# Kernel optimization log

Hardware: AMD Instinct MI355X
Metric: run time of the kernel (lower is better)

## Reference

```python
import jax, jax.numpy as jnp
import numpy as np

N, E, IN, H, C, ED = 100000, 1600000, 128, 4, 32, 16
HC = H * C
NEG_SLOPE = 0.2
EPS = 1e-5


def setup_inputs() -> dict:
    key = jax.random.key(0)
    ks = jax.random.split(key, 12)
    x = jax.random.normal(ks[0], (N, IN), jnp.float32)
    edge_index = jax.random.randint(ks[1], (2, E), 0, N, dtype=jnp.int32)
    edge_attr = jax.random.normal(ks[2], (E, ED), jnp.float32)
    s_in = 1.0 / np.sqrt(IN)
    s_ed = 1.0 / np.sqrt(ED)
    s_c = 1.0 / np.sqrt(C)
    Wl = jax.random.normal(ks[3], (IN, HC), jnp.float32) * s_in
    bl = jnp.zeros((HC,), jnp.float32)
    Wr = jax.random.normal(ks[4], (IN, HC), jnp.float32) * s_in
    br = jnp.zeros((HC,), jnp.float32)
    We = jax.random.normal(ks[5], (ED, HC), jnp.float32) * s_ed
    att = jax.random.normal(ks[6], (H, C), jnp.float32) * s_c
    bias = jnp.zeros((HC,), jnp.float32)
    ln_weight = jnp.ones((HC,), jnp.float32)
    ln_bias = jnp.zeros((HC,), jnp.float32)
    return {"x": x, "edge_index": edge_index, "edge_attr": edge_attr,
            "Wl": Wl, "bl": bl, "Wr": Wr, "br": br, "We": We,
            "att": att, "bias": bias, "ln_weight": ln_weight, "ln_bias": ln_bias}


def gatv2_block(x, src, dst, edge_attr, Wl, bl, Wr, br, We, att, bias, ln_weight, ln_bias):
    n = x.shape[0]
    xl = (x @ Wl + bl).reshape(n, H, C)  # source-side transform
    xr = (x @ Wr + br).reshape(n, H, C)  # target-side transform
    # add_self_loops with fill_value='mean': self-loop edge_attr = mean of
    # incoming edge_attr per node (0 for isolated nodes)
    ea_sum = jax.ops.segment_sum(edge_attr, dst, num_segments=n)
    cnt = jax.ops.segment_sum(jnp.ones((edge_attr.shape[0],), edge_attr.dtype), dst, num_segments=n)
    self_attr = ea_sum / jnp.maximum(cnt, 1.0)[:, None]
    loop = jnp.arange(n, dtype=src.dtype)
    src_a = jnp.concatenate([src, loop])
    dst_a = jnp.concatenate([dst, loop])
    ea_a = jnp.concatenate([edge_attr, self_attr], axis=0)
    e_emb = (ea_a @ We).reshape(-1, H, C)
    # GATv2 attention: a^T LeakyReLU(xl_j + xr_i + e)
    m = xl[src_a] + xr[dst_a] + e_emb            # [Etot, H, C]
    m = jax.nn.leaky_relu(m, NEG_SLOPE)
    alpha = jnp.einsum('ehc,hc->eh', m, att)     # [Etot, H]
    amax = jax.ops.segment_max(alpha, dst_a, num_segments=n)
    alpha = jnp.exp(alpha - amax[dst_a])
    denom = jax.ops.segment_sum(alpha, dst_a, num_segments=n)
    alpha = alpha / denom[dst_a]
    out = jax.ops.segment_sum(xl[src_a] * alpha[:, :, None], dst_a, num_segments=n)
    h = out.reshape(n, HC) + bias
    # residual (in_dim == H*C so no projection), PyG graph-mode LayerNorm
    z = x + h
    mu = jnp.mean(z)
    var = jnp.mean((z - mu) ** 2)
    z = (z - mu) / jnp.sqrt(var + EPS)
    z = z * ln_weight + ln_bias
    return jax.nn.relu(z)  # dropout = identity in eval


def reference(x, edge_index, edge_attr, Wl, bl, Wr, br, We, att, bias, ln_weight, ln_bias):
    src, dst = edge_index[0], edge_index[1]
    return gatv2_block(x, src, dst, edge_attr, Wl, bl, Wr, br, We, att, bias, ln_weight, ln_bias)
```

## Files before the change

kernel.cpp:

```cpp
#include <hip/hip_runtime.h>
#include <hip/hip_bf16.h>

static constexpr float NEG_SLOPE = 0.2f;
static constexpr float LN_EPS = 1e-5f;

typedef float v2f __attribute__((ext_vector_type(2)));
typedef __attribute__((ext_vector_type(8))) short bf16x8;
typedef __attribute__((ext_vector_type(4))) float f32x4;

__device__ __forceinline__ unsigned f2b(float f) {
  unsigned u = __float_as_uint(f);
  return (u + 0x7fffu + ((u >> 16) & 1u)) >> 16;
}
__device__ __forceinline__ v2f b2f2(ushort2 u) {
  v2f r;
  r.x = __uint_as_float((unsigned)u.x << 16);
  r.y = __uint_as_float((unsigned)u.y << 16);
  return r;
}
__device__ __forceinline__ float sbl(unsigned w) {
  return __uint_as_float(w << 16);
}
__device__ __forceinline__ float sbh(unsigned w) {
  return __uint_as_float(w & 0xFFFF0000u);
}

__device__ __forceinline__ float head_sum16(float x) {
  float t;
  t = __int_as_float(__builtin_amdgcn_update_dpp(
      0, __float_as_int(x), 0xB1, 0xF, 0xF, true));
  x += t;
  t = __int_as_float(__builtin_amdgcn_update_dpp(
      0, __float_as_int(x), 0x4E, 0xF, 0xF, true));
  x += t;
  t = __int_as_float(__builtin_amdgcn_update_dpp(
      0, __float_as_int(x), 0x124, 0xF, 0xF, true));
  x += t;
  t = __int_as_float(__builtin_amdgcn_update_dpp(
      0, __float_as_int(x), 0x128, 0xF, 0xF, true));
  x += t;
  return x;
}

__global__ __launch_bounds__(256) void k_packB(
    const float* __restrict__ Wl, const float* __restrict__ Wr,
    const float* __restrict__ bl, const float* __restrict__ br,
    ushort* __restrict__ Bpack, float* __restrict__ bcat,
    int* __restrict__ degcur, int N2, int* __restrict__ tot,
    int* __restrict__ src_pad, double* __restrict__ red)
{
  int tid = blockIdx.x * 256 + threadIdx.x;
  int l = tid & 63, s = (tid >> 6) & 3, t = tid >> 8;
  int col = t * 16 + (l & 15);
  int kb = s * 32 + (l >> 4) * 8;
  const float* __restrict__ W = (col < 128) ? Wl : Wr;
  int c = col & 127;
  unsigned p[4];
#pragma unroll
  for (int i = 0; i < 4; ++i) {
    unsigned lo = f2b(W[(size_t)(kb + 2 * i) * 128 + c]);
    unsigned hi = f2b(W[(size_t)(kb + 2 * i + 1) * 128 + c]);
    p[i] = lo | (hi << 16);
  }
  *(uint4*)(Bpack + (size_t)tid * 8) = make_uint4(p[0], p[1], p[2], p[3]);
  if (tid < 256) bcat[tid] = (tid < 128) ? bl[tid] : br[tid - 128];
  if (tid < 8) src_pad[tid] = 0;
  if (tid < 2) red[tid] = 0.0;
  if (tid == 0) *tot = 0;
  for (int i = tid; i < N2; i += 4096) degcur[i] = 0;
}

__global__ __launch_bounds__(256) void k_gemm_mfma(
    const float* __restrict__ x, const ushort* __restrict__ Bpack,
    const float* __restrict__ bcat, ushort* __restrict__ xl,
    float* __restrict__ outz, int n, const int* __restrict__ dst,
    int* __restrict__ deg, int E)
{
  const int lane = threadIdx.x & 63;
  const int w = threadIdx.x >> 6;
  const int row0 = blockIdx.x * 64 + w * 16;
  const int rowA = min(row0 + (lane & 15), n - 1);
  const int kgrp = lane >> 4;

  f32x4 acc[16];
#pragma unroll
  for (int t = 0; t < 16; ++t) acc[t] = (f32x4){0.f, 0.f, 0.f, 0.f};

#pragma unroll
  for (int s = 0; s < 4; ++s) {
    const float4* ap =
        (const float4*)(x + (size_t)rowA * 128 + s * 32 + kgrp * 8);
    float4 a0 = ap[0], a1 = ap[1];
    bf16x8 a;
    a[0] = (short)f2b(a0.x); a[1] = (short)f2b(a0.y);
    a[2] = (short)f2b(a0.z); a[3] = (short)f2b(a0.w);
    a[4] = (short)f2b(a1.x); a[5] = (short)f2b(a1.y);
    a[6] = (short)f2b(a1.z); a[7] = (short)f2b(a1.w);
#pragma unroll
    for (int t = 0; t < 16; ++t) {
      bf16x8 b =
          *(const bf16x8*)(Bpack + (((size_t)t * 4 + s) * 64 + lane) * 8);
      acc[t] = __builtin_amdgcn_mfma_f32_16x16x32_bf16(a, b, acc[t], 0, 0, 0);
    }
  }

  const int colg = lane & 15;
  const int rbase = row0 + (lane >> 4) * 4;
#pragma unroll
  for (int t = 0; t < 16; ++t) {
    const int col = t * 16 + colg;
    const float bia = bcat[col];
    if (col < 128) {
#pragma unroll
      for (int r = 0; r < 4; ++r) {
        const int R = rbase + r;
        if (R < n) xl[(size_t)R * 128 + col] = (ushort)f2b(acc[t][r] + bia);
      }
    } else {
      const int c = col - 128;
#pragma unroll
      for (int r = 0; r < 4; ++r) {
        const int R = rbase + r;
        if (R < n) outz[(size_t)R * 128 + c] = acc[t][r] + bia;
      }
    }
  }

  for (int e = blockIdx.x * 256 + threadIdx.x; e < E; e += gridDim.x * 256)
    atomicAdd(&deg[dst[e]], 1);
}

__global__ __launch_bounds__(256) void k_allocscan(
    const int* __restrict__ deg, int* __restrict__ offs, int* __restrict__ tot,
    int n)
{
  __shared__ int s[256];
  __shared__ int base;
  const int b = blockIdx.x, t = threadIdx.x, i = b * 256 + t;
  const int v = (i < n) ? deg[i] : 0;
  s[t] = v;
  __syncthreads();
  for (int o = 1; o < 256; o <<= 1) {
    int u = (t >= o) ? s[t - o] : 0;
    __syncthreads();
    s[t] += u;
    __syncthreads();
  }
  if (t == 255) base = atomicAdd(tot, s[255]);
  __syncthreads();
  if (i < n) offs[i] = base + s[t] - v;
}

__global__ __launch_bounds__(256) void k_fill(
    const int* __restrict__ src, const int* __restrict__ dst,
    const int* __restrict__ offs, int* __restrict__ cursor,
    const float4* __restrict__ ea4, int* __restrict__ csr_src,
    ushort* __restrict__ csr_ea, int E)
{
  int e = blockIdx.x * 256 + threadIdx.x;
  if (e >= E) return;
  int d = dst[e];
  int pos = offs[d] + atomicAdd(&cursor[d], 1);
  csr_src[pos] = src[e];
  float4 r0 = ea4[(size_t)e * 4 + 0], r1 = ea4[(size_t)e * 4 + 1];
  float4 r2 = ea4[(size_t)e * 4 + 2], r3 = ea4[(size_t)e * 4 + 3];
  uint4* o4 = (uint4*)(csr_ea + (size_t)pos * 16);
  o4[0] = make_uint4(f2b(r0.x) | (f2b(r0.y) << 16), f2b(r0.z) | (f2b(r0.w) << 16),
                     f2b(r1.x) | (f2b(r1.y) << 16), f2b(r1.z) | (f2b(r1.w) << 16));
  o4[1] = make_uint4(f2b(r2.x) | (f2b(r2.y) << 16), f2b(r2.z) | (f2b(r2.w) << 16),
                     f2b(r3.x) | (f2b(r3.y) << 16), f2b(r3.z) | (f2b(r3.w) << 16));
}

__global__ __launch_bounds__(256) void k_fused(
    const int* __restrict__ csr_src, const ushort* __restrict__ csr_ea,
    const int* __restrict__ offs, const int* __restrict__ deg,
    const ushort* __restrict__ xl, const float* __restrict__ We,
    const float* __restrict__ att, const float* __restrict__ x,
    const float* __restrict__ bias, float* __restrict__ outz,
    double* __restrict__ red, int N)
{
  const int lane = threadIdx.x & 63;
  const int wv = threadIdx.x >> 6;
  const int gw = __builtin_amdgcn_readfirstlane(blockIdx.x * 4 + wv);
  const int nw = gridDim.x * 4;
  const uint* __restrict__ eaD = (const uint*)csr_ea;
  const v2f* __restrict__ We2 = (const v2f*)We;
  const v2f* __restrict__ X2 = (const v2f*)x;
  v2f* __restrict__ Z2 = (v2f*)outz;

  __shared__ float sEA[4][2][256];
  float* const myEA = &sEA[wv][0][0];

  v2f we[16];
#pragma unroll
  for (int k = 0; k < 16; ++k) we[k] = We2[k * 64 + lane];
  const v2f a2 = ((const v2f*)att)[lane];
  const v2f b2 = ((const v2f*)bias)[lane];

  float sred = 0.f, s2red = 0.f;

  int node = gw;
  int beg = 0, len = 0;
  if (node < N) {
    beg = offs[node];
    len = deg[node];
  }
  uint d0 = 0, d1 = 0;
  if (node < N && len > 0) {
    const uint* p = eaD + (size_t)beg * 8;
    d0 = p[lane];
    d1 = p[lane + 64];
  }

  while (node < N) {
    const int nodeN = node + nw;
    int begN = 0, lenN = 0;
    if (nodeN < N) {
      begN = offs[nodeN];
      lenN = deg[nodeN];
    }

    const v2f xrv = Z2[(size_t)node * 64 + lane];
    const v2f xvSelf =
        b2f2(*(const ushort2*)(xl + (size_t)node * 128 + 2 * lane));

    float den = 0.f;
    v2f acc = {0.f, 0.f}, embsum = {0.f, 0.f};

    int buf = 0;
    if (len > 0) {
      float2* dst = (float2*)myEA;
      dst[lane] = make_float2(sbl(d0), sbh(d0));
      dst[lane + 64] = make_float2(sbl(d1), sbh(d1));
    }
    const int nchunk = (len + 15) >> 4;

    int g = beg;
    v2f xvCur = {0.f, 0.f};
    int sN = 0;
    if (len > 0) {
      const int s0 = csr_src[beg];
      xvCur = b2f2(*(const ushort2*)(xl + (size_t)s0 * 128 + 2 * lane));
      sN = csr_src[beg + 1];
    }

    for (int c = 0; c < nchunk; ++c) {
      if (c + 1 < nchunk) {
        const uint* p = eaD + (size_t)(beg + (c + 1) * 16) * 8;
        d0 = p[lane];
        d1 = p[lane + 64];
      } else if (nodeN < N && lenN > 0) {
        const uint* p = eaD + (size_t)begN * 8;
        d0 = p[lane];
        d1 = p[lane + 64];
      }
      const int m = min(16, len - c * 16);
      const float* eb = myEA + buf * 256;
      for (int i = 0; i < m; ++i) {
        const float4 q0 = *(const float4*)(eb + i * 16);
        const float4 q1 = *(const float4*)(eb + i * 16 + 4);
        const float4 q2 = *(const float4*)(eb + i * 16 + 8);
        const float4 q3 = *(const float4*)(eb + i * 16 + 12);
        const v2f xvN =
            b2f2(*(const ushort2*)(xl + (size_t)sN * 128 + 2 * lane));
        const int sNN = csr_src[g + 2];
        v2f u0 = q0.x * we[0];
        v2f u1 = q0.y * we[1];
        v2f u2 = q0.z * we[2];
        v2f u3 = q0.w * we[3];
        u0 += q1.x * we[4];
        u1 += q1.y * we[5];
        u2 += q1.z * we[6];
        u3 += q1.w * we[7];
        u0 += q2.x * we[8];
        u1 += q2.y * we[9];
        u2 += q2.z * we[10];
        u3 += q2.w * we[11];
        u0 += q3.x * we[12];
        u1 += q3.y * we[13];
        u2 += q3.z * we[14];
        u3 += q3.w * we[15];
        const v2f emb = (u0 + u1) + (u2 + u3);
        embsum += emb;
        v2f mm = xvCur + xrv + emb;
        v2f ml;
        ml.x = fmaxf(mm.x, NEG_SLOPE * mm.x);
        ml.y = fmaxf(mm.y, NEG_SLOPE * mm.y);
        const float part = head_sum16(fmaf(ml.y, a2.y, ml.x * a2.x));
        const float p = __expf(part);
        den += p;
        acc += xvCur * p;
        xvCur = xvN;
        sN = sNN;
        ++g;
      }
      if (c + 1 < nchunk) {
        float2* dst = (float2*)(myEA + (buf ^ 1) * 256);
        dst[lane] = make_float2(sbl(d0), sbh(d0));
        dst[lane + 64] = make_float2(sbl(d1), sbh(d1));
        buf ^= 1;
      }
    }
    if (nchunk == 0 && nodeN < N && lenN > 0) {
      const uint* p = eaD + (size_t)begN * 8;
      d0 = p[lane];
      d1 = p[lane + 64];
    }

    {
      const float inv = (len > 0) ? 1.f / (float)len : 0.f;
      const v2f embS = embsum * inv;
      v2f mm = xvSelf + xrv + embS;
      v2f ml;
      ml.x = fmaxf(mm.x, NEG_SLOPE * mm.x);
      ml.y = fmaxf(mm.y, NEG_SLOPE * mm.y);
      const float part = head_sum16(fmaf(ml.y, a2.y, ml.x * a2.x));
      const float p = __expf(part);
      den += p;
      acc += xvSelf * p;
    }

    const float invden = 1.f / den;
    const float o0 = acc.x * invden;
    const float o1 = acc.y * invden;

    const v2f xvn = X2[(size_t)node * 64 + lane];
    const float v0 = xvn.x + o0 + b2.x;
    const float v1 = xvn.y + o1 + b2.y;
    Z2[(size_t)node * 64 + lane] = (v2f){v0, v1};
    sred += v0 + v1;
    s2red += v0 * v0 + v1 * v1;

    node = nodeN;
    beg = begN;
    len = lenN;
  }

#pragma unroll
  for (int o = 32; o > 0; o >>= 1) {
    sred += __shfl_down(sred, o);
    s2red += __shfl_down(s2red, o);
  }
  __shared__ double ls[4], ls2[4];
  if ((threadIdx.x & 63) == 0) {
    ls[wv] = (double)sred;
    ls2[wv] = (double)s2red;
  }
  __syncthreads();
  if (threadIdx.x == 0) {
    unsafeAtomicAdd(red, ls[0] + ls[1] + ls[2] + ls[3]);
    unsafeAtomicAdd(red + 1, ls2[0] + ls2[1] + ls2[2] + ls2[3]);
  }
}

__global__ __launch_bounds__(256) void k_final(
    float* __restrict__ z, const double* __restrict__ red,
    const float* __restrict__ lnw, const float* __restrict__ lnb, int M4)
{
  int i = blockIdx.x * 256 + threadIdx.x;
  if (i >= M4) return;
  const double invM = 1.0 / ((double)M4 * 4.0);
  const double mu = red[0] * invM;
  const double var = red[1] * invM - mu * mu;
  const float sc = rsqrtf((float)var + LN_EPS);
  const float muf = (float)mu;
  const float4* W4 = (const float4*)lnw;
  const float4* L4 = (const float4*)lnb;
  float4* Z4 = (float4*)z;
  float4 zv = Z4[i], wv = W4[i & 31], lv = L4[i & 31];
  float4 o;
  o.x = fmaxf((zv.x - muf) * sc * wv.x + lv.x, 0.f);
  o.y = fmaxf((zv.y - muf) * sc * wv.y + lv.y, 0.f);
  o.z = fmaxf((zv.z - muf) * sc * wv.z + lv.z, 0.f);
  o.w = fmaxf((zv.w - muf) * sc * wv.w + lv.w, 0.f);
  Z4[i] = o;
}

extern "C" void kernel_launch(void* const* d_in, const int* in_sizes, int n_in,
                              void* d_out, int out_size, void* d_ws,
                              size_t ws_size, hipStream_t stream)
{
  const float* x = (const float*)d_in[0];
  const int* ei = (const int*)d_in[1];
  const float* edge_attr = (const float*)d_in[2];
  const float* Wl = (const float*)d_in[3];
  const float* bl = (const float*)d_in[4];
  const float* Wr = (const float*)d_in[5];
  const float* br = (const float*)d_in[6];
  const float* We = (const float*)d_in[7];
  const float* att = (const float*)d_in[8];
  const float* bias = (const float*)d_in[9];
  const float* lnw = (const float*)d_in[10];
  const float* lnb = (const float*)d_in[11];
  float* out = (float*)d_out;

  const int N = in_sizes[0] / 128;
  const int E = in_sizes[1] / 2;
  const int M = N * 128;
  const int* srcp = ei;
  const int* dstp = ei + E;
  const int nb = (N + 255) / 256;

  ushort* xl = (ushort*)d_ws;
  int* deg = (int*)(xl + (size_t)M);
  int* cursor = deg + N;
  int* offs = cursor + N;
  int* tot = offs + N;
  int* csr_src = tot + 8;
  ushort* csr_ea =
      (ushort*)((((size_t)(csr_src + E + 8)) + 63) & ~(size_t)63);
  double* red = (double*)(
      (((size_t)(csr_ea + (size_t)E * 16 + 512)) + 127) & ~(size_t)127);
  ushort* Bpack = (ushort*)(red + 8);
  float* bcat = (float*)(Bpack + 4096 * 8);

  k_packB<<<16, 256, 0, stream>>>(Wl, Wr, bl, br, Bpack, bcat, deg, 2 * N,
                                  tot, csr_src + E, red);
  k_gemm_mfma<<<(N + 63) / 64, 256, 0, stream>>>(x, Bpack, bcat, xl, out, N,
                                                 dstp, deg, E);
  k_allocscan<<<nb, 256, 0, stream>>>(deg, offs, tot, N);
  k_fill<<<(E + 255) / 256, 256, 0, stream>>>(srcp, dstp, offs, cursor,
                                              (const float4*)edge_attr,
                                              csr_src, csr_ea, E);
  k_fused<<<2048, 256, 0, stream>>>(csr_src, csr_ea, offs, deg, xl, We, att,
                                    x, bias, out, red, N);
  k_final<<<(M / 4 + 255) / 256, 256, 0, stream>>>(out, red, lnw, lnb, M / 4);
}
```

Before: 493.3 us.

## Compute edge embeddings with bf16 MFMA over padded 16-edge CSR chunks

Pads each node's CSR segment to a multiple of 16 and stores edge attributes in MFMA A-fragment layout. The fused kernel then computes each chunk's 16x128 edge embedding with bf16 MFMA into LDS instead of per-edge scalar FMAs. The source-row prefetch is also deepened to two edges ahead. This costs extra padded storage, a memset of the CSR buffers, and an LDS round trip, and it wastes half the MFMA K dimension.

```diff
diff --git a/kernel.cpp b/kernel.cpp
--- a/kernel.cpp
+++ b/kernel.cpp
@@ -17,12 +17,6 @@
   r.x = __uint_as_float((unsigned)u.x << 16);
   r.y = __uint_as_float((unsigned)u.y << 16);
   return r;
-}
-__device__ __forceinline__ float sbl(unsigned w) {
-  return __uint_as_float(w << 16);
-}
-__device__ __forceinline__ float sbh(unsigned w) {
-  return __uint_as_float(w & 0xFFFF0000u);
 }
 
 __device__ __forceinline__ float head_sum16(float x) {
@@ -47,7 +41,7 @@
     const float* __restrict__ bl, const float* __restrict__ br,
     ushort* __restrict__ Bpack, float* __restrict__ bcat,
     int* __restrict__ degcur, int N2, int* __restrict__ tot,
-    int* __restrict__ src_pad, double* __restrict__ red)
+    double* __restrict__ red)
 {
   int tid = blockIdx.x * 256 + threadIdx.x;
   int l = tid & 63, s = (tid >> 6) & 3, t = tid >> 8;
@@ -64,7 +58,6 @@
   }
   *(uint4*)(Bpack + (size_t)tid * 8) = make_uint4(p[0], p[1], p[2], p[3]);
   if (tid < 256) bcat[tid] = (tid < 128) ? bl[tid] : br[tid - 128];
-  if (tid < 8) src_pad[tid] = 0;
   if (tid < 2) red[tid] = 0.0;
   if (tid == 0) *tot = 0;
   for (int i = tid; i < N2; i += 4096) degcur[i] = 0;
@@ -137,7 +130,7 @@
   __shared__ int s[256];
   __shared__ int base;
   const int b = blockIdx.x, t = threadIdx.x, i = b * 256 + t;
-  const int v = (i < n) ? deg[i] : 0;
+  const int v = (i < n) ? ((deg[i] + 15) & ~15) : 0;
   s[t] = v;
   __syncthreads();
   for (int o = 1; o < 256; o <<= 1) {
@@ -155,7 +148,7 @@
     const int* __restrict__ src, const int* __restrict__ dst,
     const int* __restrict__ offs, int* __restrict__ cursor,
     const float4* __restrict__ ea4, int* __restrict__ csr_src,
-    ushort* __restrict__ csr_ea, int E)
+    uint4* __restrict__ csr_ea4, int E)
 {
   int e = blockIdx.x * 256 + threadIdx.x;
   if (e >= E) return;
@@ -164,11 +157,13 @@
   csr_src[pos] = src[e];
   float4 r0 = ea4[(size_t)e * 4 + 0], r1 = ea4[(size_t)e * 4 + 1];
   float4 r2 = ea4[(size_t)e * 4 + 2], r3 = ea4[(size_t)e * 4 + 3];
-  uint4* o4 = (uint4*)(csr_ea + (size_t)pos * 16);
-  o4[0] = make_uint4(f2b(r0.x) | (f2b(r0.y) << 16), f2b(r0.z) | (f2b(r0.w) << 16),
-                     f2b(r1.x) | (f2b(r1.y) << 16), f2b(r1.z) | (f2b(r1.w) << 16));
-  o4[1] = make_uint4(f2b(r2.x) | (f2b(r2.y) << 16), f2b(r2.z) | (f2b(r2.w) << 16),
-                     f2b(r3.x) | (f2b(r3.y) << 16), f2b(r3.z) | (f2b(r3.w) << 16));
+  const int chunk = pos >> 4, r = pos & 15;
+  csr_ea4[(size_t)chunk * 32 + r] =
+      make_uint4(f2b(r0.x) | (f2b(r0.y) << 16), f2b(r0.z) | (f2b(r0.w) << 16),
+                 f2b(r1.x) | (f2b(r1.y) << 16), f2b(r1.z) | (f2b(r1.w) << 16));
+  csr_ea4[(size_t)chunk * 32 + r + 16] =
+      make_uint4(f2b(r2.x) | (f2b(r2.y) << 16), f2b(r2.z) | (f2b(r2.w) << 16),
+                 f2b(r3.x) | (f2b(r3.y) << 16), f2b(r3.z) | (f2b(r3.w) << 16));
 }
 
 __global__ __launch_bounds__(256) void k_fused(
@@ -183,17 +178,28 @@
   const int wv = threadIdx.x >> 6;
   const int gw = __builtin_amdgcn_readfirstlane(blockIdx.x * 4 + wv);
   const int nw = gridDim.x * 4;
-  const uint* __restrict__ eaD = (const uint*)csr_ea;
-  const v2f* __restrict__ We2 = (const v2f*)We;
   const v2f* __restrict__ X2 = (const v2f*)x;
   v2f* __restrict__ Z2 = (v2f*)outz;
 
-  __shared__ float sEA[4][2][256];
-  float* const myEA = &sEA[wv][0][0];
-
-  v2f we[16];
-#pragma unroll
-  for (int k = 0; k < 16; ++k) we[k] = We2[k * 64 + lane];
+  __shared__ float sEmb[4][16 * 128];
+  float* const myEmb = sEmb[wv];
+
+  bf16x8 weB[8];
+  {
+    const int colb = lane & 15;
+    const int k0 = (lane >> 4) * 8;
+#pragma unroll
+    for (int t = 0; t < 8; ++t) {
+      bf16x8 b;
+#pragma unroll
+      for (int i = 0; i < 8; ++i) {
+        const int k = k0 + i;
+        b[i] = (k < 16) ? (short)f2b(We[(size_t)k * 128 + t * 16 + colb])
+                        : (short)0;
+      }
+      weB[t] = b;
+    }
+  }
   const v2f a2 = ((const v2f*)att)[lane];
   const v2f b2 = ((const v2f*)bias)[lane];
 
@@ -205,12 +211,9 @@
     beg = offs[node];
     len = deg[node];
   }
-  uint d0 = 0, d1 = 0;
-  if (node < N && len > 0) {
-    const uint* p = eaD + (size_t)beg * 8;
-    d0 = p[lane];
-    d1 = p[lane + 64];
-  }
+  uint4 afrag = {0, 0, 0, 0};
+  if (node < N && len > 0 && lane < 32)
+    afrag = *(const uint4*)(csr_ea + ((size_t)(beg >> 4) * 32 + lane) * 8);
 
   while (node < N) {
     const int nodeN = node + nw;
@@ -226,91 +229,72 @@
 
     float den = 0.f;
     v2f acc = {0.f, 0.f}, embsum = {0.f, 0.f};
-
-    int buf = 0;
+    const int nchunk = (len + 15) >> 4;
+    const int c0 = beg >> 4;
+
+    int g = beg;
+    v2f xv0 = {0.f, 0.f}, xv1 = {0.f, 0.f};
+    int s2 = 0;
     if (len > 0) {
-      float2* dst = (float2*)myEA;
-      dst[lane] = make_float2(sbl(d0), sbh(d0));
-      dst[lane + 64] = make_float2(sbl(d1), sbh(d1));
-    }
-    const int nchunk = (len + 15) >> 4;
-
-    int g = beg;
-    v2f xvCur = {0.f, 0.f};
-    int sN = 0;
-    if (len > 0) {
-      const int s0 = csr_src[beg];
-      xvCur = b2f2(*(const ushort2*)(xl + (size_t)s0 * 128 + 2 * lane));
-      sN = csr_src[beg + 1];
+      const int sa = csr_src[beg];
+      xv0 = b2f2(*(const ushort2*)(xl + (size_t)sa * 128 + 2 * lane));
+      const int sb = csr_src[beg + 1];
+      xv1 = b2f2(*(const ushort2*)(xl + (size_t)sb * 128 + 2 * lane));
+      s2 = csr_src[beg + 2];
     }
 
     for (int c = 0; c < nchunk; ++c) {
-      if (c + 1 < nchunk) {
-        const uint* p = eaD + (size_t)(beg + (c + 1) * 16) * 8;
-        d0 = p[lane];
-        d1 = p[lane + 64];
-      } else if (nodeN < N && lenN > 0) {
-        const uint* p = eaD + (size_t)begN * 8;
-        d0 = p[lane];
-        d1 = p[lane + 64];
+      uint4 afragN = {0, 0, 0, 0};
+      if (lane < 32) {
+        if (c + 1 < nchunk)
+          afragN =
+              *(const uint4*)(csr_ea + ((size_t)(c0 + c + 1) * 32 + lane) * 8);
+        else if (lenN > 0)
+          afragN =
+              *(const uint4*)(csr_ea + ((size_t)(begN >> 4) * 32 + lane) * 8);
+      }
+      {
+        const int colb = lane & 15;
+        const int row4 = (lane >> 4) * 4;
+        const bf16x8 a = *(const bf16x8*)&afrag;
+#pragma unroll
+        for (int t = 0; t < 8; ++t) {
+          f32x4 cf = __builtin_amdgcn_mfma_f32_16x16x32_bf16(
+              a, weB[t], (f32x4){0.f, 0.f, 0.f, 0.f}, 0, 0, 0);
+#pragma unroll
+          for (int q = 0; q < 4; ++q)
+            myEmb[(row4 + q) * 128 + t * 16 + colb] = cf[q];
+        }
       }
       const int m = min(16, len - c * 16);
-      const float* eb = myEA + buf * 256;
       for (int i = 0; i < m; ++i) {
-        const float4 q0 = *(const float4*)(eb + i * 16);
-        const float4 q1 = *(const float4*)(eb + i * 16 + 4);
-        const float4 q2 = *(const float4*)(eb + i * 16 + 8);
-        const float4 q3 = *(const float4*)(eb + i * 16 + 12);
-        const v2f xvN =
-            b2f2(*(const ushort2*)(xl + (size_t)sN * 128 + 2 * lane));
-        const int sNN = csr_src[g + 2];
-        v2f u0 = q0.x * we[0];
-        v2f u1 = q0.y * we[1];
-        v2f u2 = q0.z * we[2];
-        v2f u3 = q0.w * we[3];
-        u0 += q1.x * we[4];
-        u1 += q1.y * we[5];
-        u2 += q1.z * we[6];
-        u3 += q1.w * we[7];
-        u0 += q2.x * we[8];
-        u1 += q2.y * we[9];
-        u2 += q2.z * we[10];
-        u3 += q2.w * we[11];
-        u0 += q3.x * we[12];
-        u1 += q3.y * we[13];
-        u2 += q3.z * we[14];
-        u3 += q3.w * we[15];
-        const v2f emb = (u0 + u1) + (u2 + u3);
+        const v2f emb = *(const v2f*)(myEmb + i * 128 + 2 * lane);
+        const v2f xv2 =
+            b2f2(*(const ushort2*)(xl + (size_t)s2 * 128 + 2 * lane));
+        const int s3 = csr_src[g + 3];
         embsum += emb;
-        v2f mm = xvCur + xrv + emb;
+        v2f mm = (xv0 + emb) + xrv;
         v2f ml;
         ml.x = fmaxf(mm.x, NEG_SLOPE * mm.x);
         ml.y = fmaxf(mm.y, NEG_SLOPE * mm.y);
         const float part = head_sum16(fmaf(ml.y, a2.y, ml.x * a2.x));
         const float p = __expf(part);
         den += p;
-        acc += xvCur * p;
-        xvCur = xvN;
-        sN = sNN;
+        acc += xv0 * p;
+        xv0 = xv1;
+        xv1 = xv2;
+        s2 = s3;
         ++g;
       }
-      if (c + 1 < nchunk) {
-        float2* dst = (float2*)(myEA + (buf ^ 1) * 256);
-        dst[lane] = make_float2(sbl(d0), sbh(d0));
-        dst[lane + 64] = make_float2(sbl(d1), sbh(d1));
-        buf ^= 1;
-      }
-    }
-    if (nchunk == 0 && nodeN < N && lenN > 0) {
-      const uint* p = eaD + (size_t)begN * 8;
-      d0 = p[lane];
-      d1 = p[lane + 64];
-    }
+      afrag = afragN;
+    }
+    if (nchunk == 0 && lenN > 0 && lane < 32)
+      afrag = *(const uint4*)(csr_ea + ((size_t)(begN >> 4) * 32 + lane) * 8);
 
     {
       const float inv = (len > 0) ? 1.f / (float)len : 0.f;
       const v2f embS = embsum * inv;
-      v2f mm = xvSelf + xrv + embS;
+      v2f mm = (xvSelf + embS) + xrv;
       v2f ml;
       ml.x = fmaxf(mm.x, NEG_SLOPE * mm.x);
       ml.y = fmaxf(mm.y, NEG_SLOPE * mm.y);
@@ -400,6 +384,7 @@
   const int* srcp = ei;
   const int* dstp = ei + E;
   const int nb = (N + 255) / 256;
+  const size_t SLOTS = (size_t)E + 15 * (size_t)N + 16;
 
   ushort* xl = (ushort*)d_ws;
   int* deg = (int*)(xl + (size_t)M);
@@ -408,20 +393,22 @@
   int* tot = offs + N;
   int* csr_src = tot + 8;
   ushort* csr_ea =
-      (ushort*)((((size_t)(csr_src + E + 8)) + 63) & ~(size_t)63);
+      (ushort*)((((size_t)(csr_src + SLOTS + 8)) + 63) & ~(size_t)63);
   double* red = (double*)(
-      (((size_t)(csr_ea + (size_t)E * 16 + 512)) + 127) & ~(size_t)127);
+      (((size_t)(csr_ea + SLOTS * 16 + 64)) + 127) & ~(size_t)127);
   ushort* Bpack = (ushort*)(red + 8);
   float* bcat = (float*)(Bpack + 4096 * 8);
 
+  hipMemsetAsync(csr_src, 0, (SLOTS + 8) * sizeof(int), stream);
+
   k_packB<<<16, 256, 0, stream>>>(Wl, Wr, bl, br, Bpack, bcat, deg, 2 * N,
-                                  tot, csr_src + E, red);
+                                  tot, red);
   k_gemm_mfma<<<(N + 63) / 64, 256, 0, stream>>>(x, Bpack, bcat, xl, out, N,
                                                  dstp, deg, E);
   k_allocscan<<<nb, 256, 0, stream>>>(deg, offs, tot, N);
   k_fill<<<(E + 255) / 256, 256, 0, stream>>>(srcp, dstp, offs, cursor,
                                               (const float4*)edge_attr,
-                                              csr_src, csr_ea, E);
+                                              csr_src, (uint4*)csr_ea, E);
   k_fused<<<2048, 256, 0, stream>>>(csr_src, csr_ea, offs, deg, xl, We, att,
                                     x, bias, out, red, N);
   k_final<<<(M / 4 + 255) / 256, 256, 0, stream>>>(out, red, lnw, lnb, M / 4);
```

New measurement: 548.6 us. +11.2%, slower.
